# Optimization experiments

Hardware: AMD Instinct MI355X
Metric: run time of the kernel (lower is better)

The kernel has to match this reference:

```python
import jax, jax.numpy as jnp
import numpy as np

N_EMBEDS = 1024
N_HEADS = 16
HEAD_DIM = N_EMBEDS // N_HEADS
SCALE = HEAD_DIM ** (-0.5)
B, T = 2, 2048


def setup_inputs() -> dict:
    key = jax.random.key(0)
    k1, k2, k3, k4 = jax.random.split(key, 4)
    x = jax.random.normal(k1, (B, T, N_EMBEDS), dtype=jnp.float32)
    # Glorot-uniform-style init like keras Dense defaults (scale irrelevant for correctness)
    w_qkv = jax.random.normal(k2, (N_EMBEDS, 3 * N_EMBEDS), dtype=jnp.float32) * (N_EMBEDS ** -0.5)
    w_proj = jax.random.normal(k3, (N_EMBEDS, N_EMBEDS), dtype=jnp.float32) * (N_EMBEDS ** -0.5)
    b_proj = jnp.zeros((N_EMBEDS,), dtype=jnp.float32)
    return {"x": x, "w_qkv": w_qkv, "w_proj": w_proj, "b_proj": b_proj}


def reference(x, w_qkv, w_proj, b_proj):
    Bc, Tc, D = x.shape
    qkv = x @ w_qkv                                   # [B,T,3D]
    q, k, v = jnp.split(qkv, 3, axis=-1)
    def heads(t):
        return t.reshape(Bc, Tc, N_HEADS, HEAD_DIM).transpose(0, 2, 1, 3)  # [B,H,T,hd]
    q, k, v = heads(q), heads(k), heads(v)
    att = jnp.einsum("bhqd,bhkd->bhqk", q, k) * SCALE  # [B,H,T,T]
    causal = jnp.tril(jnp.ones((Tc, Tc), dtype=bool))[None, None]
    att = jnp.where(causal, att, jnp.float32(-1e9))
    att = jax.nn.softmax(att, axis=-1)
    out = jnp.einsum("bhqk,bhkd->bhqd", att, v)        # [B,H,T,hd]
    out = out.transpose(0, 2, 1, 3).reshape(Bc, Tc, D)
    return out @ w_proj + b_proj
```

## Files before the change

kernel.cpp:

```cpp
#include <hip/hip_runtime.h>
#include <hip/hip_bf16.h>


typedef __bf16 bf16;
typedef float f32x4 __attribute__((ext_vector_type(4)));
typedef float f32x16 __attribute__((ext_vector_type(16)));
typedef bf16 bf16x4 __attribute__((ext_vector_type(4)));
typedef bf16 bf16x8 __attribute__((ext_vector_type(8)));

#define B_ 2
#define T_ 2048
#define D_ 1024
#define H_ 16
#define HD_ 64
#define QSPLIT 9

__device__ __forceinline__ f32x16 mfma32(bf16x8 a, bf16x8 b, f32x16 c) {
    return __builtin_amdgcn_mfma_f32_32x32x16_bf16(a, b, c, 0, 0, 0);
}

__device__ __forceinline__ void gload16(void* l, const void* g) {
    __builtin_amdgcn_global_load_lds(
        (const __attribute__((address_space(1))) unsigned int*)g,
        (__attribute__((address_space(3))) unsigned int*)l, 16, 0, 0);
}

__device__ __forceinline__ f32x16 z16() {
    f32x16 v;
#pragma unroll
    for (int i = 0; i < 16; ++i) v[i] = 0.f;
    return v;
}

__global__ __launch_bounds__(256) void cast_f32_bf16(const float* __restrict__ in,
                                                     bf16* __restrict__ out, int n4) {
    int i = blockIdx.x * 256 + threadIdx.x;
    if (i < n4) {
        float4 v = ((const float4*)in)[i];
        bf16x4 o = { (bf16)v.x, (bf16)v.y, (bf16)v.z, (bf16)v.w };
        ((bf16x4*)out)[i] = o;
    }
}

__global__ __launch_bounds__(256) void cast_transpose(const float* __restrict__ in,
                                                      bf16* __restrict__ out, int R, int C) {
    __shared__ float tile[32][33];
    int cx = blockIdx.x * 32 + threadIdx.x;
    int r0 = blockIdx.y * 32;
#pragma unroll
    for (int j = 0; j < 32; j += 8)
        tile[threadIdx.y + j][threadIdx.x] = in[(size_t)(r0 + threadIdx.y + j) * C + cx];
    __syncthreads();
    int rx = r0 + threadIdx.x;
    int c0 = blockIdx.x * 32;
#pragma unroll
    for (int j = 0; j < 32; j += 8)
        out[(size_t)(c0 + threadIdx.y + j) * R + rx] = (bf16)tile[threadIdx.x][threadIdx.y + j];
}

template <int MW, int NWN, int EPI>
__global__ __launch_bounds__(256) void gemm_k(
    const bf16* __restrict__ A, const bf16* __restrict__ Bt,
    int M, int N, int K,
    bf16* __restrict__ qb, bf16* __restrict__ kb, bf16* __restrict__ vt,
    const float* __restrict__ bias, float* __restrict__ outf) {
    constexpr int BM = 64 * MW;
    constexpr int BN = 64 * NWN;
    __shared__ bf16 sA[BM * 64];
    __shared__ bf16 sB[BN * 64];
    const int tid = threadIdx.x;
    const int wave = tid >> 6, lane = tid & 63;
    const int ln = lane & 31, hi = lane >> 5;
    const int wr = (wave >> 1) * (32 * MW);
    const int wc = (wave & 1) * (32 * NWN);
    const int m0 = blockIdx.x * BM, n0 = blockIdx.y * BN;

    f32x16 acc[MW][NWN];
#pragma unroll
    for (int mi = 0; mi < MW; ++mi)
#pragma unroll
        for (int ni = 0; ni < NWN; ++ni) acc[mi][ni] = z16();

    for (int k0 = 0; k0 < K; k0 += 64) {
        __syncthreads();
#pragma unroll
        for (int j = 0; j < 2 * MW; ++j) {
            int c = tid + 256 * j;
            int r = c >> 3, g = (c & 7) ^ (r & 7);
            gload16(&sA[c * 8], A + (size_t)(m0 + r) * K + k0 + 8 * g);
        }
#pragma unroll
        for (int j = 0; j < 2 * NWN; ++j) {
            int c = tid + 256 * j;
            int r = c >> 3, g = (c & 7) ^ (r & 7);
            gload16(&sB[c * 8], Bt + (size_t)(n0 + r) * K + k0 + 8 * g);
        }
        __syncthreads();
#pragma unroll
        for (int s = 0; s < 4; ++s) {
            bf16x8 av[MW], bv[NWN];
#pragma unroll
            for (int mi = 0; mi < MW; ++mi) {
                int r = wr + mi * 32 + ln;
                av[mi] = *(const bf16x8*)((const char*)sA + r * 128 +
                                          ((((s << 1) | hi) ^ (r & 7)) << 4));
            }
#pragma unroll
            for (int ni = 0; ni < NWN; ++ni) {
                int r = wc + ni * 32 + ln;
                bv[ni] = *(const bf16x8*)((const char*)sB + r * 128 +
                                          ((((s << 1) | hi) ^ (r & 7)) << 4));
            }
#pragma unroll
            for (int mi = 0; mi < MW; ++mi)
#pragma unroll
                for (int ni = 0; ni < NWN; ++ni)
                    acc[mi][ni] = mfma32(av[mi], bv[ni], acc[mi][ni]);
        }
    }

#pragma unroll
    for (int mi = 0; mi < MW; ++mi)
#pragma unroll
        for (int ni = 0; ni < NWN; ++ni) {
            int col = n0 + wc + ni * 32 + ln;
            if (EPI == 0) {
                int part = col >> 10, h = (col >> 6) & 15, d = col & 63;
                if (part == 2) {
#pragma unroll
                    for (int g4 = 0; g4 < 4; ++g4) {
                        int row = m0 + wr + mi * 32 + 8 * g4 + 4 * hi;
                        int bb = row >> 11, tt = row & (T_ - 1);
                        bf16x4 w;
#pragma unroll
                        for (int j = 0; j < 4; ++j)
                            w[j] = (bf16)acc[mi][ni][4 * g4 + j];
                        *(bf16x4*)&vt[(((size_t)(bb * H_ + h) * HD_) + d) * T_ + tt] = w;
                    }
                } else {
                    bf16* dst = (part == 0) ? qb : kb;
#pragma unroll
                    for (int r = 0; r < 16; ++r) {
                        int row = m0 + wr + mi * 32 + (r & 3) + 8 * (r >> 2) + 4 * hi;
                        int bb = row >> 11, tt = row & (T_ - 1);
                        dst[((size_t)(bb * H_ + h) * T_ + tt) * HD_ + d] =
                            (bf16)acc[mi][ni][r];
                    }
                }
            } else {
#pragma unroll
                for (int r = 0; r < 16; ++r) {
                    int row = m0 + wr + mi * 32 + (r & 3) + 8 * (r >> 2) + 4 * hi;
                    outf[(size_t)row * N + col] = acc[mi][ni][r] + bias[col];
                }
            }
        }
}

__device__ __forceinline__ bf16x8 kread(const char* base, int row, int s, int hi) {
    int b = (row * 128 + s * 32 + hi * 16) ^ ((row & 7) << 4);
    return *(const bf16x8*)(base + b);
}
__device__ __forceinline__ bf16x8 vread(const char* base, int row, int s, int hi) {
    int sw = (row & 7) << 4;
    int b0 = (row * 128 + s * 32 + hi * 8) ^ sw;
    int b1 = (row * 128 + s * 32 + hi * 8 + 16) ^ sw;
    bf16x4 lo = *(const bf16x4*)(base + b0);
    bf16x4 hi4 = *(const bf16x4*)(base + b1);
    return __builtin_shufflevector(lo, hi4, 0, 1, 2, 3, 4, 5, 6, 7);
}

__global__ __launch_bounds__(256, 3) void attn_kernel(
    const bf16* __restrict__ qb, const bf16* __restrict__ kb,
    const bf16* __restrict__ vtb, bf16* __restrict__ ob,
    bf16* __restrict__ oP, float2* __restrict__ mlP) {
    __shared__ bf16 sK2[2][4096];
    __shared__ bf16 sV2[2][4096];

    const int bid = blockIdx.x;
    const int bh = bid & 31;
    const int sid = bid >> 5;
    int qt, seg, t0, t1;
    if (sid < QSPLIT) {
        qt = sid; seg = -1; t0 = 0; t1 = 2 * qt + 2;
    } else {
        int idx = sid - QSPLIT;
        qt = QSPLIT + (idx >> 1);
        seg = idx & 1;
        if (seg == 0) { t0 = 0; t1 = qt + 1; }
        else          { t0 = qt + 1; t1 = 2 * qt + 2; }
    }
    const int b = bh >> 4, h = bh & 15;
    const int tid = threadIdx.x, wave = tid >> 6, lane = tid & 63;
    const int ln = lane & 31, hi = lane >> 5;
    const int qs = qt * 128 + wave * 32;
    const int qrow = qs + ln;

    const bf16* Qg = qb + (size_t)bh * (T_ * HD_);
    const bf16* Kg = kb + (size_t)bh * (T_ * HD_);
    const bf16* Vtg = vtb + (size_t)bh * (HD_ * T_);

    bf16x8 qf[4];
#pragma unroll
    for (int s = 0; s < 4; ++s) {
        bf16x8 v = *(const bf16x8*)&Qg[(size_t)qrow * HD_ + s * 16 + hi * 8];
#pragma unroll
        for (int e = 0; e < 8; ++e) v[e] = (bf16)((float)v[e] * 0.1803368801f);
        qf[s] = v;
    }
    bf16x8 ones;
#pragma unroll
    for (int e = 0; e < 8; ++e) ones[e] = (bf16)1.0f;

    const int rr0 = tid >> 3;
    const int gg = ((tid & 7) ^ (rr0 & 7)) * 8;

    {
        int kv0 = t0 * 64;
        gload16(&sK2[0][tid * 8], Kg + (size_t)(kv0 + rr0) * HD_ + gg);
        gload16(&sK2[0][(tid + 256) * 8], Kg + (size_t)(kv0 + rr0 + 32) * HD_ + gg);
        gload16(&sV2[0][tid * 8], Vtg + (size_t)rr0 * T_ + kv0 + gg);
        gload16(&sV2[0][(tid + 256) * 8], Vtg + (size_t)(rr0 + 32) * T_ + kv0 + gg);
    }
    __syncthreads();

    const float NINF = -__builtin_inff();
    f32x16 oA = z16(), oB = z16();
    float mR = NINF, lR = 0.f;
    int cur = 0;

    for (int t = t0; t < t1; ++t) {
        if ((t + 1) < t1) {
            int kv0 = (t + 1) * 64;
            bf16* kd = sK2[cur ^ 1];
            bf16* vd = sV2[cur ^ 1];
            gload16(&kd[tid * 8], Kg + (size_t)(kv0 + rr0) * HD_ + gg);
            gload16(&kd[(tid + 256) * 8], Kg + (size_t)(kv0 + rr0 + 32) * HD_ + gg);
            gload16(&vd[tid * 8], Vtg + (size_t)rr0 * T_ + kv0 + gg);
            gload16(&vd[(tid + 256) * 8], Vtg + (size_t)(rr0 + 32) * T_ + kv0 + gg);
        }

        if (64 * t <= qs + 31) {
            const char* kbase = (const char*)sK2[cur];
            const char* vbase = (const char*)sV2[cur];

            f32x16 p0 = z16(), p1 = z16();
            __builtin_amdgcn_s_setprio(1);
#pragma unroll
            for (int s = 0; s < 4; ++s) {
                bf16x8 a0 = kread(kbase, ln, s, hi);
                bf16x8 a1 = kread(kbase, ln + 32, s, hi);
                p0 = mfma32(a0, qf[s], p0);
                p1 = mfma32(a1, qf[s], p1);
            }
            __builtin_amdgcn_s_setprio(0);

            if (64 * t + 63 > qs) {
                int kvb = 64 * t + 4 * hi;
#pragma unroll
                for (int r = 0; r < 16; ++r) {
                    int kvr = kvb + (r & 3) + 8 * (r >> 2);
                    if (kvr > qrow) p0[r] = NINF;
                    if (kvr + 32 > qrow) p1[r] = NINF;
                }
            }

            float mx0 = NINF, mx1 = NINF, mx2 = NINF, mx3 = NINF;
#pragma unroll
            for (int r = 0; r < 16; r += 4) {
                mx0 = fmaxf(fmaxf(p0[r], p1[r]), mx0);
                mx1 = fmaxf(fmaxf(p0[r + 1], p1[r + 1]), mx1);
                mx2 = fmaxf(fmaxf(p0[r + 2], p1[r + 2]), mx2);
                mx3 = fmaxf(fmaxf(p0[r + 3], p1[r + 3]), mx3);
            }
            float pm = fmaxf(fmaxf(mx0, mx1), fmaxf(mx2, mx3));
            pm = fmaxf(pm, __shfl_xor(pm, 32));

            if (__any(pm > mR + 8.f)) {
                float mnew = fmaxf(mR, pm);
                float fac = exp2f(mR - mnew);
                lR *= fac;
#pragma unroll
                for (int r = 0; r < 16; ++r) { oA[r] *= fac; oB[r] *= fac; }
                mR = mnew;
            }

            bf16x8 pa0, pa1, pa2, pa3;
#pragma unroll
            for (int e = 0; e < 8; ++e) {
                pa0[e] = (bf16)exp2f(p0[e] - mR);
                pa1[e] = (bf16)exp2f(p0[8 + e] - mR);
                pa2[e] = (bf16)exp2f(p1[e] - mR);
                pa3[e] = (bf16)exp2f(p1[8 + e] - mR);
            }

            __builtin_amdgcn_s_setprio(1);
            f32x16 sacc = mfma32(ones, pa0, z16());
            sacc = mfma32(ones, pa1, sacc);
            sacc = mfma32(ones, pa2, sacc);
            sacc = mfma32(ones, pa3, sacc);
#pragma unroll
            for (int s = 0; s < 4; ++s) {
                bf16x8 pas = (s == 0) ? pa0 : (s == 1) ? pa1 : (s == 2) ? pa2 : pa3;
                oA = mfma32(vread(vbase, ln, s, hi), pas, oA);
                oB = mfma32(vread(vbase, ln + 32, s, hi), pas, oB);
            }
            __builtin_amdgcn_s_setprio(0);
            lR += sacc[0];
        }

        __syncthreads();
        cur ^= 1;
    }

    if (seg < 0) {
        float inv = 1.f / lR;
        bf16* orow = ob + ((size_t)(b * T_ + qrow)) * D_ + h * HD_;
#pragma unroll
        for (int g = 0; g < 4; ++g) {
            bf16x4 w, w2;
#pragma unroll
            for (int j = 0; j < 4; ++j) {
                w[j] = (bf16)(oA[4 * g + j] * inv);
                w2[j] = (bf16)(oB[4 * g + j] * inv);
            }
            *(bf16x4*)&orow[4 * hi + 8 * g] = w;
            *(bf16x4*)&orow[32 + 4 * hi + 8 * g] = w2;
        }
    } else {
        int row = wave * 32 + ln;
        size_t sbase = (((size_t)bh * (16 - QSPLIT) + (qt - QSPLIT)) * 2 + seg);
        bf16* prow = oP + (sbase * 128 + row) * 64;
#pragma unroll
        for (int g = 0; g < 4; ++g) {
            bf16x4 w, w2;
#pragma unroll
            for (int j = 0; j < 4; ++j) {
                w[j] = (bf16)oA[4 * g + j];
                w2[j] = (bf16)oB[4 * g + j];
            }
            *(bf16x4*)&prow[4 * hi + 8 * g] = w;
            *(bf16x4*)&prow[32 + 4 * hi + 8 * g] = w2;
        }
        if (hi == 0) mlP[sbase * 128 + row] = make_float2(mR, lR);
    }
}

__global__ __launch_bounds__(256) void attn_merge(
    const bf16* __restrict__ oP, const float2* __restrict__ mlP,
    bf16* __restrict__ ob) {
    constexpr int NQS = 16 - QSPLIT;
    int gid = blockIdx.x * 256 + threadIdx.x;
    int bh = gid / (NQS * 128);
    int rem = gid - bh * (NQS * 128);
    int qi = rem >> 7, row = rem & 127;
    int b = bh >> 4, h = bh & 15;
    int t = (QSPLIT + qi) * 128 + row;
    size_t sbase = ((size_t)bh * NQS + qi) * 2;
    float2 ml0 = mlP[(sbase + 0) * 128 + row];
    float2 ml1 = mlP[(sbase + 1) * 128 + row];
    float ms = fmaxf(ml0.x, ml1.x);
    float w0 = exp2f(ml0.x - ms), w1 = exp2f(ml1.x - ms);
    float inv = 1.f / (ml0.y * w0 + ml1.y * w1);
    w0 *= inv; w1 *= inv;
    const bf16* r0 = oP + ((sbase + 0) * 128 + row) * 64;
    const bf16* r1 = oP + ((sbase + 1) * 128 + row) * 64;
    bf16* dst = ob + ((size_t)(b * T_ + t)) * D_ + h * HD_;
#pragma unroll
    for (int g = 0; g < 8; ++g) {
        bf16x8 a = *(const bf16x8*)&r0[g * 8];
        bf16x8 c = *(const bf16x8*)&r1[g * 8];
        bf16x8 o;
#pragma unroll
        for (int j = 0; j < 8; ++j)
            o[j] = (bf16)((float)a[j] * w0 + (float)c[j] * w1);
        *(bf16x8*)&dst[g * 8] = o;
    }
}

extern "C" void kernel_launch(void* const* d_in, const int* in_sizes, int n_in,
                              void* d_out, int out_size, void* d_ws, size_t ws_size,
                              hipStream_t stream) {
    const float* x = (const float*)d_in[0];
    const float* w_qkv = (const float*)d_in[1];
    const float* w_proj = (const float*)d_in[2];
    const float* b_proj = (const float*)d_in[3];
    float* out = (float*)d_out;
    char* ws = (char*)d_ws;

    bf16* xb = (bf16*)(ws);
    bf16* ob = (bf16*)(ws);
    bf16* wqkvt = (bf16*)(ws + 8388608);
    bf16* oP = (bf16*)(ws + 8388608);
    float2* mlP = (float2*)(ws + 15728640);
    bf16* qbuf = (bf16*)(ws + 16777216);
    bf16* kbuf = (bf16*)(ws + 25165824);
    bf16* wprojt = (bf16*)(ws + 25165824);
    bf16* vtbuf = (bf16*)(ws + 33554432);

    cast_f32_bf16<<<4096, 256, 0, stream>>>(x, xb, (B_ * T_ * D_) / 4);
    dim3 tb(32, 8);
    cast_transpose<<<dim3(3 * D_ / 32, D_ / 32), tb, 0, stream>>>(w_qkv, wqkvt, D_, 3 * D_);

    gemm_k<2, 2, 0><<<dim3((B_ * T_) / 128, (3 * D_) / 128), 256, 0, stream>>>(
        xb, wqkvt, B_ * T_, 3 * D_, D_, qbuf, kbuf, vtbuf, nullptr, nullptr);

    attn_kernel<<<23 * 32, 256, 0, stream>>>(qbuf, kbuf, vtbuf, ob, oP, mlP);
    attn_merge<<<112, 256, 0, stream>>>(oP, mlP, ob);

    cast_transpose<<<dim3(D_ / 32, D_ / 32), tb, 0, stream>>>(w_proj, wprojt, D_, D_);

    gemm_k<1, 2, 1><<<dim3((B_ * T_) / 64, D_ / 128), 256, 0, stream>>>(
        ob, wprojt, B_ * T_, D_, D_, nullptr, nullptr, nullptr, b_proj, out);
}
```

Baseline: 118.6 us.

## Fuse prep casts into one launch, reorder attention blocks, write seg0 partial directly

Merges the x cast and both weight cast-transposes into a single prep kernel, so two launches go away and the w_proj transpose moves ahead of the attention. Attention block-to-work assignment now comes from lookup tables that put the longest query tiles first, for better load balance across CUs. The first segment of split rows writes its unnormalized output straight into the final buffer, and the merge reads it back from there, which cuts partial-buffer traffic. The workspace layout is rearranged so wprojt no longer aliases kbuf.

Result: faster. 110.6 us (-6.7%).

```diff
diff --git a/kernel.cpp b/kernel.cpp
--- a/kernel.cpp
+++ b/kernel.cpp
@@ -32,30 +32,43 @@
     return v;
 }
 
-__global__ __launch_bounds__(256) void cast_f32_bf16(const float* __restrict__ in,
-                                                     bf16* __restrict__ out, int n4) {
-    int i = blockIdx.x * 256 + threadIdx.x;
-    if (i < n4) {
-        float4 v = ((const float4*)in)[i];
+__global__ __launch_bounds__(256) void prep(
+    const float* __restrict__ x, bf16* __restrict__ xb,
+    const float* __restrict__ wqkv, bf16* __restrict__ wqkvt,
+    const float* __restrict__ wproj, bf16* __restrict__ wprojt) {
+    __shared__ float tile[32][33];
+    const int bid = blockIdx.x;
+    const int tid = threadIdx.x;
+    if (bid < 4096) {
+        int i = bid * 256 + tid;
+        float4 v = ((const float4*)x)[i];
         bf16x4 o = { (bf16)v.x, (bf16)v.y, (bf16)v.z, (bf16)v.w };
-        ((bf16x4*)out)[i] = o;
-    }
-}
-
-__global__ __launch_bounds__(256) void cast_transpose(const float* __restrict__ in,
-                                                      bf16* __restrict__ out, int R, int C) {
-    __shared__ float tile[32][33];
-    int cx = blockIdx.x * 32 + threadIdx.x;
-    int r0 = blockIdx.y * 32;
+        ((bf16x4*)xb)[i] = o;
+        return;
+    }
+    const float* in;
+    bf16* outp;
+    int C, bx, by;
+    if (bid < 4096 + 3072) {
+        int r = bid - 4096;
+        in = wqkv; outp = wqkvt; C = 3 * D_; bx = r % 96; by = r / 96;
+    } else {
+        int r = bid - 7168;
+        in = wproj; outp = wprojt; C = D_; bx = r % 32; by = r / 32;
+    }
+    const int R = D_;
+    const int tx = tid & 31, ty = tid >> 5;
+    int cx = bx * 32 + tx;
+    int r0 = by * 32;
 #pragma unroll
     for (int j = 0; j < 32; j += 8)
-        tile[threadIdx.y + j][threadIdx.x] = in[(size_t)(r0 + threadIdx.y + j) * C + cx];
+        tile[ty + j][tx] = in[(size_t)(r0 + ty + j) * C + cx];
     __syncthreads();
-    int rx = r0 + threadIdx.x;
-    int c0 = blockIdx.x * 32;
+    int rx = r0 + tx;
+    int c0 = bx * 32;
 #pragma unroll
     for (int j = 0; j < 32; j += 8)
-        out[(size_t)(c0 + threadIdx.y + j) * R + rx] = (bf16)tile[threadIdx.x][threadIdx.y + j];
+        outp[(size_t)(c0 + ty + j) * R + rx] = (bf16)tile[tx][ty + j];
 }
 
 template <int MW, int NWN, int EPI>
@@ -157,6 +170,13 @@
         }
 }
 
+static __device__ const signed char QT_T[23] = {
+    8, 7, 15, 15, 14, 14, 6, 13, 10, 10, 5, 11, 11, 12, 12, 13,
+    0, 1, 2, 3, 4, 9, 9};
+static __device__ const signed char SEG_T[23] = {
+    -1, -1, 0, 1, 0, 1, -1, 0, 0, 1, -1, 0, 1, 0, 1, 1,
+    -1, -1, -1, -1, -1, 0, 1};
+
 __device__ __forceinline__ bf16x8 kread(const char* base, int row, int s, int hi) {
     int b = (row * 128 + s * 32 + hi * 16) ^ ((row & 7) << 4);
     return *(const bf16x8*)(base + b);
@@ -180,16 +200,12 @@
     const int bid = blockIdx.x;
     const int bh = bid & 31;
     const int sid = bid >> 5;
-    int qt, seg, t0, t1;
-    if (sid < QSPLIT) {
-        qt = sid; seg = -1; t0 = 0; t1 = 2 * qt + 2;
-    } else {
-        int idx = sid - QSPLIT;
-        qt = QSPLIT + (idx >> 1);
-        seg = idx & 1;
-        if (seg == 0) { t0 = 0; t1 = qt + 1; }
-        else          { t0 = qt + 1; t1 = 2 * qt + 2; }
-    }
+    const int qt = QT_T[sid];
+    const int seg = SEG_T[sid];
+    int t0, t1;
+    if (seg < 0)       { t0 = 0;      t1 = 2 * qt + 2; }
+    else if (seg == 0) { t0 = 0;      t1 = qt + 1; }
+    else               { t0 = qt + 1; t1 = 2 * qt + 2; }
     const int b = bh >> 4, h = bh & 15;
     const int tid = threadIdx.x, wave = tid >> 6, lane = tid & 63;
     const int ln = lane & 31, hi = lane >> 5;
@@ -329,8 +345,13 @@
         }
     } else {
         int row = wave * 32 + ln;
-        size_t sbase = (((size_t)bh * (16 - QSPLIT) + (qt - QSPLIT)) * 2 + seg);
-        bf16* prow = oP + (sbase * 128 + row) * 64;
+        bf16* prow;
+        if (seg == 0) {
+            prow = ob + ((size_t)(b * T_ + qrow)) * D_ + h * HD_;
+        } else {
+            size_t sbase = (size_t)bh * (16 - QSPLIT) + (qt - QSPLIT);
+            prow = oP + (sbase * 128 + row) * 64;
+        }
 #pragma unroll
         for (int g = 0; g < 4; ++g) {
             bf16x4 w, w2;
@@ -342,7 +363,9 @@
             *(bf16x4*)&prow[4 * hi + 8 * g] = w;
             *(bf16x4*)&prow[32 + 4 * hi + 8 * g] = w2;
         }
-        if (hi == 0) mlP[sbase * 128 + row] = make_float2(mR, lR);
+        if (hi == 0)
+            mlP[(((size_t)bh * (16 - QSPLIT) + (qt - QSPLIT)) * 2 + seg) * 128 + row] =
+                make_float2(mR, lR);
     }
 }
 
@@ -356,19 +379,18 @@
     int qi = rem >> 7, row = rem & 127;
     int b = bh >> 4, h = bh & 15;
     int t = (QSPLIT + qi) * 128 + row;
-    size_t sbase = ((size_t)bh * NQS + qi) * 2;
-    float2 ml0 = mlP[(sbase + 0) * 128 + row];
-    float2 ml1 = mlP[(sbase + 1) * 128 + row];
+    size_t sbase = (size_t)bh * NQS + qi;
+    float2 ml0 = mlP[(sbase * 2 + 0) * 128 + row];
+    float2 ml1 = mlP[(sbase * 2 + 1) * 128 + row];
     float ms = fmaxf(ml0.x, ml1.x);
     float w0 = exp2f(ml0.x - ms), w1 = exp2f(ml1.x - ms);
     float inv = 1.f / (ml0.y * w0 + ml1.y * w1);
     w0 *= inv; w1 *= inv;
-    const bf16* r0 = oP + ((sbase + 0) * 128 + row) * 64;
-    const bf16* r1 = oP + ((sbase + 1) * 128 + row) * 64;
     bf16* dst = ob + ((size_t)(b * T_ + t)) * D_ + h * HD_;
+    const bf16* r1 = oP + (sbase * 128 + row) * 64;
 #pragma unroll
     for (int g = 0; g < 8; ++g) {
-        bf16x8 a = *(const bf16x8*)&r0[g * 8];
+        bf16x8 a = *(const bf16x8*)&dst[g * 8];
         bf16x8 c = *(const bf16x8*)&r1[g * 8];
         bf16x8 o;
 #pragma unroll
@@ -392,15 +414,13 @@
     bf16* ob = (bf16*)(ws);
     bf16* wqkvt = (bf16*)(ws + 8388608);
     bf16* oP = (bf16*)(ws + 8388608);
-    float2* mlP = (float2*)(ws + 15728640);
+    float2* mlP = (float2*)(ws + 12058624);
+    bf16* wprojt = (bf16*)(ws + 14680064);
     bf16* qbuf = (bf16*)(ws + 16777216);
     bf16* kbuf = (bf16*)(ws + 25165824);
-    bf16* wprojt = (bf16*)(ws + 25165824);
     bf16* vtbuf = (bf16*)(ws + 33554432);
 
-    cast_f32_bf16<<<4096, 256, 0, stream>>>(x, xb, (B_ * T_ * D_) / 4);
-    dim3 tb(32, 8);
-    cast_transpose<<<dim3(3 * D_ / 32, D_ / 32), tb, 0, stream>>>(w_qkv, wqkvt, D_, 3 * D_);
+    prep<<<8192, 256, 0, stream>>>(x, xb, w_qkv, wqkvt, w_proj, wprojt);
 
     gemm_k<2, 2, 0><<<dim3((B_ * T_) / 128, (3 * D_) / 128), 256, 0, stream>>>(
         xb, wqkvt, B_ * T_, 3 * D_, D_, qbuf, kbuf, vtbuf, nullptr, nullptr);
@@ -408,8 +428,6 @@
     attn_kernel<<<23 * 32, 256, 0, stream>>>(qbuf, kbuf, vtbuf, ob, oP, mlP);
     attn_merge<<<112, 256, 0, stream>>>(oP, mlP, ob);
 
-    cast_transpose<<<dim3(D_ / 32, D_ / 32), tb, 0, stream>>>(w_proj, wprojt, D_, D_);
-
     gemm_k<1, 2, 1><<<dim3((B_ * T_) / 64, D_ / 128), 256, 0, stream>>>(
         ob, wprojt, B_ * T_, D_, D_, nullptr, nullptr, nullptr, b_proj, out);
 }
```
